# Performance work log

Hardware: AMD Instinct MI355X
Metric: run time of the kernel (lower is better)

## Reference

```python
import jax, jax.numpy as jnp
import numpy as np

B, S, T = 64, 128, 64
HD, VS, VT = 1024, 32000, 32000


def setup_inputs() -> dict:
    key = jax.random.key(0)
    ks = jax.random.split(key, 20)
    p = lambda k, shape: (jax.random.normal(k, shape, jnp.float32) * 0.02)
    return {
        "src_nums": jax.random.randint(ks[0], (B, S), 0, VS, dtype=jnp.int32),
        "tgt_nums": jax.random.randint(ks[1], (B, T), 0, VT, dtype=jnp.int32),
        "src_emb": p(ks[2], (VS, HD)),
        "tgt_emb": p(ks[3], (VT, HD)),
        "enc_Wx1": p(ks[4], (HD, 4 * HD)),
        "enc_Wh1": p(ks[5], (HD, 4 * HD)),
        "enc_b1": jnp.zeros((4 * HD,), jnp.float32),
        "enc_Wx2": p(ks[6], (HD, 4 * HD)),
        "enc_Wh2": p(ks[7], (HD, 4 * HD)),
        "enc_b2": jnp.zeros((4 * HD,), jnp.float32),
        "dec_Wx": p(ks[8], (HD, 4 * HD)),
        "dec_Wh": p(ks[9], (HD, 4 * HD)),
        "dec_b": jnp.zeros((4 * HD,), jnp.float32),
        "dec_h0": p(ks[10], (1, HD)),
        "dec_m0": p(ks[11], (1, HD)),
        "Wt": p(ks[12], (2 * HD, HD)),
        "bt": jnp.zeros((HD,), jnp.float32),
        "Wo": p(ks[13], (HD, VT)),
        "bo": jnp.zeros((VT,), jnp.float32),
    }


def _lstm_cell(x, h, c, Wx, Wh, b):
    g = x @ Wx + h @ Wh + b            # [B, 4H], gate order i,f,g,o
    i, f, gg, o = jnp.split(g, 4, axis=-1)
    c = jax.nn.sigmoid(f) * c + jax.nn.sigmoid(i) * jnp.tanh(gg)
    h = jax.nn.sigmoid(o) * jnp.tanh(c)
    return h, c


def reference(src_nums, tgt_nums, src_emb, tgt_emb,
              enc_Wx1, enc_Wh1, enc_b1, enc_Wx2, enc_Wh2, enc_b2,
              dec_Wx, dec_Wh, dec_b, dec_h0, dec_m0, Wt, bt, Wo, bo):
    Bb, Ss = src_nums.shape
    Hd = src_emb.shape[1]
    # ---- Encoder: 2-layer LSTM over source ----
    embs = src_emb[src_nums]                       # [B,S,H]
    z0 = jnp.zeros((Bb, Hd), embs.dtype)

    def enc_step(carry, x):
        h1, c1, h2, c2 = carry
        h1, c1 = _lstm_cell(x, h1, c1, enc_Wx1, enc_Wh1, enc_b1)
        h2, c2 = _lstm_cell(h1, h2, c2, enc_Wx2, enc_Wh2, enc_b2)
        return (h1, c1, h2, c2), h2

    _, Hseq = jax.lax.scan(enc_step, (z0, z0, z0, z0), jnp.swapaxes(embs, 0, 1))
    Henc = jnp.swapaxes(Hseq, 0, 1)                # [B,S,H]
    mask = src_nums == 0                           # pad mask
    scale = 1.0 / jnp.sqrt(jnp.array(Hd, jnp.float32))

    # ---- Decoder: per-step attention + LSTMCell + tanh proj + log-softmax ----
    h = jnp.tile(dec_h0, (Bb, 1))
    m = jnp.tile(dec_m0, (Bb, 1))

    def dec_step(carry, tgt):
        h, m, loss = carry
        scores = jnp.einsum('bd,bsd->bs', h, Henc) * scale
        scores = jnp.where(mask, -jnp.inf, scores)
        a = jax.nn.softmax(scores, axis=-1)
        ctx = jnp.einsum('bs,bsd->bd', a, Henc)
        z = jnp.tanh(jnp.concatenate([ctx, h], axis=-1) @ Wt + bt)
        logp = jax.nn.log_softmax(z @ Wo + bo, axis=-1)    # [B,V]
        tok_lp = jnp.take_along_axis(logp, tgt[:, None], axis=-1)[:, 0]
        loss = loss - jnp.sum(jnp.where(tgt != 0, tok_lp, 0.0))
        x = tgt_emb[tgt]
        h, m = _lstm_cell(x, h, m, dec_Wx, dec_Wh, dec_b)
        return (h, m, loss), None

    (_, _, loss), _ = jax.lax.scan(
        dec_step, (h, m, jnp.float32(0.0)), jnp.swapaxes(tgt_nums, 0, 1))
    return loss
```

## Files before the change

### kernel.cpp

```cpp
#include <hip/hip_runtime.h>


#define Bv 64
#define Sv 128
#define Tv 64
#define Hv 1024
#define H4v 4096
#define Vv 32000
#define NBLK 256
#define ROUNDS 129

using bf16x8 = __attribute__((ext_vector_type(8))) short;
using f32x4  = __attribute__((ext_vector_type(4))) float;

typedef __attribute__((address_space(1))) const void gvoid_t;
typedef __attribute__((address_space(3))) void lvoid_t;

__device__ __forceinline__ void gload16(const void* g, void* l) {
  __builtin_amdgcn_global_load_lds((gvoid_t*)g, (lvoid_t*)l, 16, 0, 0);
}

__device__ __forceinline__ float bf2f(unsigned short u) {
  unsigned int v = ((unsigned int)u) << 16;
  return __uint_as_float(v);
}
__device__ __forceinline__ unsigned short f2bf(float f) {
  unsigned int u = __float_as_uint(f);
  return (unsigned short)((u + 0x7FFFu + ((u >> 16) & 1u)) >> 16);
}
__device__ __forceinline__ float sigm(float x) { return 1.f / (1.f + __expf(-x)); }
__device__ __forceinline__ float tanh_f(float x) {
  float ax = fabsf(x);
  float e = __expf(-2.f * ax);
  float t = (1.f - e) / (1.f + e);
  return copysignf(t, x);
}

__device__ __forceinline__ int4 ldx4(const unsigned short* p) {
  int4 r;
  asm volatile("global_load_dwordx4 %0, %1, off" : "=v"(r) : "v"(p));
  return r;
}
__device__ __forceinline__ unsigned ldu16(const unsigned short* p) {
  unsigned r;
  asm volatile("global_load_ushort %0, %1, off" : "=v"(r) : "v"(p));
  return r;
}
__device__ __forceinline__ void st_u16_wt(unsigned short* p, unsigned v) {
  asm volatile("global_store_short %0, %1, off sc0 sc1" :: "v"(p), "v"(v) : "memory");
}
__device__ __forceinline__ void vm_wait(int n) {
  if (n >= 8)      asm volatile("s_waitcnt vmcnt(8)" ::: "memory");
  else if (n >= 4) asm volatile("s_waitcnt vmcnt(4)" ::: "memory");
  else             asm volatile("s_waitcnt vmcnt(0)" ::: "memory");
}

__global__ __launch_bounds__(256) void transpose_bf16(const float* __restrict__ in,
                                                      unsigned short* __restrict__ out,
                                                      int R, int C, int ostride) {
  __shared__ float tile[32][33];
  int tx = threadIdx.x, ty = threadIdx.y;
  int c0 = blockIdx.x * 32, r0 = blockIdx.y * 32;
#pragma unroll
  for (int i = 0; i < 32; i += 8)
    tile[ty + i][tx] = in[(size_t)(r0 + ty + i) * C + c0 + tx];
  __syncthreads();
#pragma unroll
  for (int i = 0; i < 32; i += 8)
    out[(size_t)(c0 + ty + i) * ostride + r0 + tx] = f2bf(tile[tx][ty + i]);
}

__global__ __launch_bounds__(256) void gather_emb(const int* __restrict__ toks,
                                                  const float* __restrict__ emb,
                                                  unsigned short* __restrict__ dst) {
  int r = blockIdx.x, tid = threadIdx.x;
  int tok = toks[r];
  int j = tid * 4;
  float4 v = *(const float4*)&emb[(size_t)tok * Hv + j];
  ushort4 o;
  o.x = f2bf(v.x); o.y = f2bf(v.y); o.z = f2bf(v.z); o.w = f2bf(v.w);
  *(ushort4*)&dst[(size_t)r * Hv + j] = o;
}

__global__ __launch_bounds__(256) void init_k(unsigned short* __restrict__ zhx,
                                              unsigned short* __restrict__ hdx0,
                                              const float* __restrict__ h0,
                                              int* __restrict__ bar) {
  int idx = blockIdx.x * 256 + threadIdx.x;
  int j = idx & (Hv - 1);
  int b = idx >> 10;
  zhx[idx] = 0;
  hdx0[(j >> 4) * 1024 + b * 16 + (j & 15)] = f2bf(h0[j]);
  if (idx < 256) bar[idx] = 0;
}

template <int EPI>
__global__ __launch_bounds__(256) void gemm128(const unsigned short* __restrict__ A,
                                               const unsigned short* __restrict__ Bt,
                                               const float* __restrict__ bias,
                                               unsigned short* __restrict__ Cbf,
                                               int M, int N, int K,
                                               float* __restrict__ partial,
                                               float* __restrict__ tlog,
                                               const int* __restrict__ tgt) {
  __shared__ unsigned short As[128 * 64];
  __shared__ unsigned short Bs[128 * 64];
  int tid = threadIdx.x, lane = tid & 63, w = tid >> 6;
  int wr = w >> 1, wc = w & 1;
  int m0 = blockIdx.y * 128, n0 = blockIdx.x * 128;
  f32x4 acc[4][4] = {};
  for (int k0 = 0; k0 < K; k0 += 64) {
    __syncthreads();
#pragma unroll
    for (int q = 0; q < 4; ++q) {
      int idx = q * 256 + tid;
      int row = idx >> 3, phys = idx & 7, lg = phys ^ (row & 7);
      gload16(A + (size_t)(m0 + row) * K + k0 + lg * 8, &As[idx * 8]);
    }
#pragma unroll
    for (int q = 0; q < 4; ++q) {
      int idx = q * 256 + tid;
      int row = idx >> 3, phys = idx & 7, lg = phys ^ (row & 7);
      gload16(Bt + (size_t)(n0 + row) * K + k0 + lg * 8, &Bs[idx * 8]);
    }
    __syncthreads();
#pragma unroll
    for (int kk = 0; kk < 64; kk += 32) {
      int lgb = (kk >> 3) + (lane >> 4);
      bf16x8 af[4], bfr[4];
#pragma unroll
      for (int m = 0; m < 4; ++m) {
        int row = wr * 64 + m * 16 + (lane & 15);
        af[m] = *(const bf16x8*)&As[(row * 8 + (lgb ^ (row & 7))) * 8];
      }
#pragma unroll
      for (int n = 0; n < 4; ++n) {
        int row = wc * 64 + n * 16 + (lane & 15);
        bfr[n] = *(const bf16x8*)&Bs[(row * 8 + (lgb ^ (row & 7))) * 8];
      }
#pragma unroll
      for (int m = 0; m < 4; ++m)
#pragma unroll
        for (int n = 0; n < 4; ++n)
          acc[m][n] = __builtin_amdgcn_mfma_f32_16x16x32_bf16(af[m], bfr[n], acc[m][n], 0, 0, 0);
    }
  }
  if (EPI != 3) {
#pragma unroll
    for (int m = 0; m < 4; ++m)
#pragma unroll
      for (int n = 0; n < 4; ++n) {
        int col = n0 + wc * 64 + n * 16 + (lane & 15);
        float bv = bias[col];
#pragma unroll
        for (int j = 0; j < 4; ++j) {
          int row = m0 + wr * 64 + m * 16 + (lane >> 4) * 4 + j;
          float v = acc[m][n][j] + bv;
          if (EPI == 2) v = tanhf(v);
          Cbf[(size_t)row * N + col] = f2bf(v);
        }
      }
  } else {
    int chunk = (n0 + wc * 64) >> 6;
#pragma unroll
    for (int m = 0; m < 4; ++m)
#pragma unroll
      for (int j = 0; j < 4; ++j) {
        int row = m0 + wr * 64 + m * 16 + (lane >> 4) * 4 + j;
        int tv = tgt[row];
        float se = 0.f;
#pragma unroll
        for (int n = 0; n < 4; ++n) {
          int col = n0 + wc * 64 + n * 16 + (lane & 15);
          float v = acc[m][n][j] + bias[col];
          se += __expf(v);
          if (col == tv) tlog[row] = v;
        }
        se += __shfl_xor(se, 1);
        se += __shfl_xor(se, 2);
        se += __shfl_xor(se, 4);
        se += __shfl_xor(se, 8);
        if ((lane & 15) == 0) partial[(size_t)chunk * M + row] = se;
      }
  }
}

__device__ __forceinline__ void gridbar(int* bar, int target, int tid, int bid) {
  __syncthreads();
  if (tid == 0)
    __hip_atomic_fetch_add(&bar[(bid & 7) * 32], 1, __ATOMIC_RELAXED, __HIP_MEMORY_SCOPE_AGENT);
  if (tid < 8) {
    int it = 0;
    while (true) {
      int s = __hip_atomic_load(&bar[tid * 32], __ATOMIC_RELAXED, __HIP_MEMORY_SCOPE_AGENT);
      s += __shfl_xor(s, 1);
      s += __shfl_xor(s, 2);
      s += __shfl_xor(s, 4);
      if (s >= target) break;
      __builtin_amdgcn_s_sleep(1);
      if (++it > (1 << 18)) break;
    }
  }
  __syncthreads();
}

template <int GRP>
__device__ __forceinline__ void run3(
    int gid, int tid, const unsigned short* __restrict__ Wg,
    const unsigned short* __restrict__ XP, const float* __restrict__ eb2,
    const float* __restrict__ m0, const unsigned short* __restrict__ ZHX,
    unsigned short* __restrict__ H1X, unsigned short* __restrict__ H2X,
    unsigned short* __restrict__ HDX, int* bar,
    unsigned short* Wl, float* gl, int bid) {
  constexpr int COLS = (GRP == 1) ? 8 : 16;
  constexpr int KD   = (GRP == 1) ? 2048 : 1024;
  constexpr int NKS  = KD / 128;
  constexpr int NFR  = (GRP == 1) ? 2 : 4;
  constexpr int TT   = (GRP == 0) ? 128 : 64;
  constexpr int GPR  = KD / 8;
  constexpr int WROWS = 4 * COLS;
  const int lane = tid & 63, w = tid >> 6, l4 = lane >> 4, l15 = lane & 15;
  const int j0 = gid * COLS;

#pragma unroll
  for (int it = 0; it < (WROWS * GPR) / 256; ++it) {
    int L = it * 256 + tid;
    int row = L / GPR;
    int g = (L % GPR) ^ (row & 7);
    int gate = row / COLS, cl = row % COLS;
    gload16(Wg + (size_t)(gate * 1024 + j0 + cl) * KD + g * 8, Wl + (size_t)L * 8);
  }
  const int rr0 = (GRP == 1) ? (tid >> 3) : (tid >> 4);
  const int cc  = (GRP == 1) ? (tid & 7) : (tid & 15);
  const bool cellact = (GRP != 1) || (tid < 128);
  float cst[4];
#pragma unroll
  for (int c = 0; c < 4; ++c) cst[c] = (GRP == 2) ? m0[j0 + cc] : 0.f;
  float br_[4];
  if (GRP == 1) {
#pragma unroll
    for (int g = 0; g < 4; ++g) br_[g] = eb2[g * 1024 + j0 + cc];
  }
  const int kq16 = w * (KD / 32);

  asm volatile("s_waitcnt vmcnt(0)" ::: "memory");
  __syncthreads();

  for (int r = 0; r < ROUNDS; ++r) {
    bool active;
    int t;
    if (GRP == 0)      { active = (r < 128); t = r; }
    else if (GRP == 1) { active = (r >= 1);  t = r - 1; }
    else               { active = (r < 63);  t = r; }
    if (active) {
      const unsigned short* slab;
      int jb;
      if (GRP == 0) {
        slab = (r == 0) ? ZHX : H1X + (size_t)(r - 1) * 65536;
        jb = w * 256;
      } else if (GRP == 2) {
        slab = HDX + (size_t)t * 65536;
        jb = w * 256;
      } else {
        if (w < 2) { slab = H1X + (size_t)(r - 1) * 65536; jb = w * 512; }
        else {
          slab = (t == 0) ? ZHX : H2X + (size_t)(t - 1) * 65536;
          jb = w * 512 - 1024;
        }
      }
      unsigned xgv[16];
      if (GRP != 1) {
#pragma unroll
        for (int c = 0; c < 4; ++c)
#pragma unroll
          for (int g = 0; g < 4; ++g)
            xgv[c * 4 + g] = ldu16(XP + ((size_t)(c * 16 + w * 4 + l4) * TT + t) * H4v +
                                   g * 1024 + j0 + l15);
      }
      const unsigned short* rp[4];
#pragma unroll
      for (int m = 0; m < 4; ++m)
        rp[m] = slab + (size_t)((jb >> 4) + (l4 >> 1)) * 1024 + (m * 16 + l15) * 16 + (l4 & 1) * 8;
      int4 afr[3][4];
#pragma unroll
      for (int pk = 0; pk < 3; ++pk)
#pragma unroll
        for (int m = 0; m < 4; ++m) afr[pk][m] = ldx4(rp[m] + pk * 2048);
      bf16x8 wb[2][NFR];
#pragma unroll
      for (int n = 0; n < NFR; ++n) {
        int row = n * 16 + l15;
        wb[0][n] = *(const bf16x8*)&Wl[(size_t)row * KD + (size_t)((kq16 + l4) ^ (row & 7)) * 8];
      }
      f32x4 acc[4][NFR] = {};
#pragma unroll
      for (int ks = 0; ks < NKS; ++ks) {
        if (ks + 1 < NKS) {
#pragma unroll
          for (int n = 0; n < NFR; ++n) {
            int row = n * 16 + l15;
            wb[(ks + 1) & 1][n] = *(const bf16x8*)&Wl[(size_t)row * KD +
                (size_t)((kq16 + (ks + 1) * 4 + l4) ^ (row & 7)) * 8];
          }
        }
        int nrem = 4 * (NKS - 1 - ks);
        vm_wait(nrem > 8 ? 8 : nrem);
        __builtin_amdgcn_sched_barrier(0);
#pragma unroll
        for (int m = 0; m < 4; ++m)
#pragma unroll
          for (int n = 0; n < NFR; ++n)
            acc[m][n] = __builtin_amdgcn_mfma_f32_16x16x32_bf16(
                *(const bf16x8*)&afr[ks % 3][m], wb[ks & 1][n], acc[m][n], 0, 0, 0);
        if (ks + 3 < NKS) {
#pragma unroll
          for (int m = 0; m < 4; ++m) afr[ks % 3][m] = ldx4(rp[m] + (ks + 3) * 2048);
        }
      }
      unsigned short* outp;
      if (GRP == 0)      outp = H1X + (size_t)r * 65536 + gid * 1024;
      else if (GRP == 2) outp = HDX + (size_t)(t + 1) * 65536 + gid * 1024;
      else               outp = H2X + (size_t)t * 65536 + (size_t)(j0 >> 4) * 1024 + (j0 & 8);
#pragma unroll
      for (int c = 0; c < 4; ++c) {
#pragma unroll
        for (int n = 0; n < NFR; ++n)
#pragma unroll
          for (int j = 0; j < 4; ++j) {
            int ric = l4 * 4 + j;
            int col = n * 16 + l15;
            gl[(w * 16 + ric) * 64 + (col ^ ((ric * 4) & 63))] = acc[c][n][j];
          }
        __syncthreads();
        if (cellact) {
          float G[4];
#pragma unroll
          for (int g = 0; g < 4; ++g) {
            int sw = (g * COLS + cc) ^ ((rr0 * 4) & 63);
            G[g] = gl[(0 * 16 + rr0) * 64 + sw] + gl[(1 * 16 + rr0) * 64 + sw] +
                   gl[(2 * 16 + rr0) * 64 + sw] + gl[(3 * 16 + rr0) * 64 + sw];
          }
          float gi, gf, gg, go;
          if (GRP == 1) {
            gi = G[0] + br_[0]; gf = G[1] + br_[1]; gg = G[2] + br_[2]; go = G[3] + br_[3];
          } else {
            gi = G[0] + bf2f((unsigned short)xgv[c * 4 + 0]);
            gf = G[1] + bf2f((unsigned short)xgv[c * 4 + 1]);
            gg = G[2] + bf2f((unsigned short)xgv[c * 4 + 2]);
            go = G[3] + bf2f((unsigned short)xgv[c * 4 + 3]);
          }
          float cn = sigm(gf) * cst[c] + sigm(gi) * tanh_f(gg);
          float hn = sigm(go) * tanh_f(cn);
          cst[c] = cn;
          st_u16_wt(outp + (c * 16 + rr0) * 16 + cc, (unsigned)f2bf(hn));
        }
        __syncthreads();
      }
      asm volatile("s_waitcnt vmcnt(0)" ::: "memory");
    }
    if (r + 1 < ROUNDS) gridbar(bar, NBLK * (r + 1), tid, bid);
  }
}

__global__ __launch_bounds__(256, 1) void chain_kernel(
    const unsigned short* __restrict__ W1T, const unsigned short* __restrict__ W2S,
    const unsigned short* __restrict__ WDT, const unsigned short* __restrict__ XP1,
    const unsigned short* __restrict__ XPD, const float* __restrict__ eb2,
    const float* __restrict__ m0, const unsigned short* __restrict__ ZHX,
    unsigned short* __restrict__ H1X, unsigned short* __restrict__ H2X,
    unsigned short* __restrict__ HDX, int* bar) {
  __shared__ unsigned short Wl[65536];
  __shared__ float gl[4 * 16 * 64];
  int bid = blockIdx.x, tid = threadIdx.x;
  if (bid < 64)
    run3<0>(bid, tid, W1T, XP1, eb2, m0, ZHX, H1X, H2X, HDX, bar, Wl, gl, bid);
  else if (bid < 192)
    run3<1>(bid - 64, tid, W2S, nullptr, eb2, m0, ZHX, H1X, H2X, HDX, bar, Wl, gl, bid);
  else
    run3<2>(bid - 192, tid, WDT, XPD, eb2, m0, ZHX, H1X, H2X, HDX, bar, Wl, gl, bid);
}

__global__ __launch_bounds__(256) void reshape_h(const unsigned short* __restrict__ H2X,
                                                 const unsigned short* __restrict__ HDX,
                                                 unsigned short* __restrict__ HENC,
                                                 unsigned short* __restrict__ HDEC) {
  int row = blockIdx.x, tid = threadIdx.x;
  int g = tid >> 2, c = (tid & 3) * 4;
  if (row < Bv * Sv) {
    int b = row >> 7, s = row & 127;
    ushort4 v = *(const ushort4*)&H2X[(size_t)s * 65536 + g * 1024 + b * 16 + c];
    *(ushort4*)&HENC[(size_t)row * Hv + tid * 4] = v;
  } else {
    int r2 = row - Bv * Sv;
    int b = r2 >> 6, t = r2 & 63;
    ushort4 v = *(const ushort4*)&HDX[(size_t)t * 65536 + g * 1024 + b * 16 + c];
    *(ushort4*)&HDEC[(size_t)r2 * Hv + tid * 4] = v;
  }
}

__global__ __launch_bounds__(256) void attn_kernel(const unsigned short* __restrict__ Hdec,
                                                   const unsigned short* __restrict__ Henc,
                                                   const int* __restrict__ src_nums,
                                                   unsigned short* __restrict__ cat) {
  __shared__ float hd[Hv];
  __shared__ float sc[Sv];
  __shared__ float al[Sv];
  __shared__ float inv_s;
  int r = blockIdx.x;
  int b = r >> 6;
  int tid = threadIdx.x;
#pragma unroll
  for (int i = 0; i < 4; ++i) {
    int j = i * 256 + tid;
    hd[j] = bf2f(Hdec[(size_t)r * Hv + j]);
  }
  __syncthreads();
  int lane = tid & 63, w = tid >> 6;
  {
    int s = w * 32 + (lane >> 1);
    int half = lane & 1;
    const unsigned short* hrow = Henc + ((size_t)(b * Sv + s)) * Hv + half * 512;
    const float* hdp = hd + half * 512;
    float ps = 0.f;
#pragma unroll 8
    for (int j = 0; j < 512; j += 2) {
      unsigned int u = *(const unsigned int*)&hrow[j];
      ps += hdp[j] * bf2f((unsigned short)(u & 0xFFFFu));
      ps += hdp[j + 1] * bf2f((unsigned short)(u >> 16));
    }
    ps += __shfl_xor(ps, 1);
    if (half == 0) {
      float v = ps * 0.03125f;
      if (src_nums[b * Sv + s] == 0) v = -1e30f;
      sc[s] = v;
    }
  }
  __syncthreads();
  if (w == 0) {
    float v0 = sc[lane], v1 = sc[lane + 64];
    float mx = fmaxf(v0, v1);
#pragma unroll
    for (int o = 1; o < 64; o <<= 1) mx = fmaxf(mx, __shfl_xor(mx, o));
    float e0 = __expf(v0 - mx), e1 = __expf(v1 - mx);
    al[lane] = e0;
    al[lane + 64] = e1;
    float ss = e0 + e1;
#pragma unroll
    for (int o = 1; o < 64; o <<= 1) ss += __shfl_xor(ss, o);
    if (lane == 0) inv_s = 1.f / ss;
  }
  __syncthreads();
  float inv = inv_s;
  int j0 = tid * 4;
  float a0 = 0, a1 = 0, a2 = 0, a3 = 0;
  for (int s2 = 0; s2 < Sv; ++s2) {
    float a = al[s2];
    const unsigned short* hr = Henc + ((size_t)(b * Sv + s2)) * Hv + j0;
    ushort4 u = *(const ushort4*)hr;
    a0 += a * bf2f(u.x);
    a1 += a * bf2f(u.y);
    a2 += a * bf2f(u.z);
    a3 += a * bf2f(u.w);
  }
  ushort4 o4;
  o4.x = f2bf(a0 * inv); o4.y = f2bf(a1 * inv); o4.z = f2bf(a2 * inv); o4.w = f2bf(a3 * inv);
  *(ushort4*)&cat[(size_t)r * 2048 + j0] = o4;
  ushort4 h4;
  h4.x = f2bf(hd[j0]); h4.y = f2bf(hd[j0 + 1]); h4.z = f2bf(hd[j0 + 2]); h4.w = f2bf(hd[j0 + 3]);
  *(ushort4*)&cat[(size_t)r * 2048 + 1024 + j0] = h4;
}

__global__ __launch_bounds__(256) void loss_row(const float* __restrict__ partial,
                                                const float* __restrict__ tlog,
                                                const int* __restrict__ tgt,
                                                float* __restrict__ rowloss) {
  int r = blockIdx.x * 256 + threadIdx.x;
  float ssum = 0.f;
  for (int c = 0; c < Vv / 64; ++c) ssum += partial[(size_t)c * (Bv * Tv) + r];
  float l = logf(ssum) - tlog[r];
  rowloss[r] = (tgt[r] != 0) ? l : 0.f;
}

__global__ __launch_bounds__(256) void loss_final(const float* __restrict__ rowloss,
                                                  float* __restrict__ out) {
  __shared__ float red[256];
  int tid = threadIdx.x;
  float s = 0.f;
  for (int i = tid; i < Bv * Tv; i += 256) s += rowloss[i];
  red[tid] = s;
  __syncthreads();
  for (int o = 128; o > 0; o >>= 1) {
    if (tid < o) red[tid] += red[tid + o];
    __syncthreads();
  }
  if (tid == 0) out[0] = red[0];
}

extern "C" void kernel_launch(void* const* d_in, const int* in_sizes, int n_in,
                              void* d_out, int out_size, void* d_ws, size_t ws_size,
                              hipStream_t stream) {
  (void)in_sizes; (void)n_in; (void)out_size; (void)ws_size;
  const int* src_nums = (const int*)d_in[0];
  const int* tgt_nums = (const int*)d_in[1];
  const float* src_emb = (const float*)d_in[2];
  const float* tgt_emb = (const float*)d_in[3];
  const float* eWx1 = (const float*)d_in[4];
  const float* eWh1 = (const float*)d_in[5];
  const float* eb1  = (const float*)d_in[6];
  const float* eWx2 = (const float*)d_in[7];
  const float* eWh2 = (const float*)d_in[8];
  const float* eb2  = (const float*)d_in[9];
  const float* dWx  = (const float*)d_in[10];
  const float* dWh  = (const float*)d_in[11];
  const float* db   = (const float*)d_in[12];
  const float* h0   = (const float*)d_in[13];
  const float* m0   = (const float*)d_in[14];
  const float* Wt   = (const float*)d_in[15];
  const float* bt   = (const float*)d_in[16];
  const float* Wo   = (const float*)d_in[17];
  const float* bo   = (const float*)d_in[18];

  char* base = (char*)d_ws;
  size_t off = 0;
  auto alloc = [&](size_t bytes) -> void* {
    void* r = base + off;
    off += (bytes + 255) & ~(size_t)255;
    return r;
  };
  unsigned short* WX1T = (unsigned short*)alloc((size_t)H4v * Hv * 2);
  unsigned short* W1T  = (unsigned short*)alloc((size_t)H4v * Hv * 2);
  unsigned short* W2S  = (unsigned short*)alloc((size_t)H4v * 2048 * 2);
  unsigned short* DWXT = (unsigned short*)alloc((size_t)H4v * Hv * 2);
  unsigned short* WDT  = (unsigned short*)alloc((size_t)H4v * Hv * 2);
  unsigned short* WTT  = (unsigned short*)alloc((size_t)Hv * 2048 * 2);
  unsigned short* WOT  = (unsigned short*)alloc((size_t)Vv * Hv * 2);
  unsigned short* SEMB = (unsigned short*)alloc((size_t)Bv * Sv * Hv * 2);
  unsigned short* TEMB = (unsigned short*)alloc((size_t)Bv * Tv * Hv * 2);
  unsigned short* XP1  = (unsigned short*)alloc((size_t)Bv * Sv * H4v * 2);
  unsigned short* XPD  = (unsigned short*)alloc((size_t)Bv * Tv * H4v * 2);
  unsigned short* HENC = (unsigned short*)alloc((size_t)Bv * Sv * Hv * 2);
  unsigned short* HDEC = (unsigned short*)alloc((size_t)Bv * Tv * Hv * 2);
  unsigned short* H1X  = (unsigned short*)alloc((size_t)Sv * Bv * Hv * 2);
  unsigned short* H2X  = (unsigned short*)alloc((size_t)Sv * Bv * Hv * 2);
  unsigned short* HDX  = (unsigned short*)alloc((size_t)Tv * Bv * Hv * 2);
  unsigned short* ZHX  = (unsigned short*)alloc((size_t)Bv * Hv * 2);
  unsigned short* CAT  = (unsigned short*)alloc((size_t)Bv * Tv * 2048 * 2);
  unsigned short* ZBUF = (unsigned short*)alloc((size_t)Bv * Tv * Hv * 2);
  float* PART  = (float*)alloc((size_t)(Vv / 64) * (Bv * Tv) * 4);
  float* TLOG  = (float*)alloc((size_t)(Bv * Tv) * 4);
  float* RLOSS = (float*)alloc((size_t)(Bv * Tv) * 4);
  int* BAR     = (int*)alloc(256 * 4);

  dim3 tb(32, 8);
  transpose_bf16<<<dim3(H4v / 32, Hv / 32), tb, 0, stream>>>(eWx1, WX1T, Hv, H4v, Hv);
  transpose_bf16<<<dim3(H4v / 32, Hv / 32), tb, 0, stream>>>(eWh1, W1T, Hv, H4v, Hv);
  transpose_bf16<<<dim3(H4v / 32, Hv / 32), tb, 0, stream>>>(eWx2, W2S, Hv, H4v, 2048);
  transpose_bf16<<<dim3(H4v / 32, Hv / 32), tb, 0, stream>>>(eWh2, W2S + 1024, Hv, H4v, 2048);
  transpose_bf16<<<dim3(H4v / 32, Hv / 32), tb, 0, stream>>>(dWx, DWXT, Hv, H4v, Hv);
  transpose_bf16<<<dim3(H4v / 32, Hv / 32), tb, 0, stream>>>(dWh, WDT, Hv, H4v, Hv);
  transpose_bf16<<<dim3(Hv / 32, 2048 / 32), tb, 0, stream>>>(Wt, WTT, 2048, Hv, 2048);
  transpose_bf16<<<dim3(Vv / 32, Hv / 32), tb, 0, stream>>>(Wo, WOT, Hv, Vv, Hv);

  init_k<<<256, 256, 0, stream>>>(ZHX, HDX, h0, BAR);
  gather_emb<<<Bv * Sv, 256, 0, stream>>>(src_nums, src_emb, SEMB);
  gather_emb<<<Bv * Tv, 256, 0, stream>>>(tgt_nums, tgt_emb, TEMB);

  gemm128<1><<<dim3(H4v / 128, (Bv * Sv) / 128), 256, 0, stream>>>(
      SEMB, WX1T, eb1, XP1, Bv * Sv, H4v, Hv, nullptr, nullptr, nullptr);
  gemm128<1><<<dim3(H4v / 128, (Bv * Tv) / 128), 256, 0, stream>>>(
      TEMB, DWXT, db, XPD, Bv * Tv, H4v, Hv, nullptr, nullptr, nullptr);

  chain_kernel<<<NBLK, 256, 0, stream>>>(W1T, W2S, WDT, XP1, XPD, eb2, m0, ZHX, H1X, H2X, HDX, BAR);

  reshape_h<<<Bv * Sv + Bv * Tv, 256, 0, stream>>>(H2X, HDX, HENC, HDEC);

  attn_kernel<<<Bv * Tv, 256, 0, stream>>>(HDEC, HENC, src_nums, CAT);
  gemm128<2><<<dim3(Hv / 128, (Bv * Tv) / 128), 256, 0, stream>>>(
      CAT, WTT, bt, ZBUF, Bv * Tv, Hv, 2048, nullptr, nullptr, nullptr);
  gemm128<3><<<dim3(Vv / 128, (Bv * Tv) / 128), 256, 0, stream>>>(
      ZBUF, WOT, bo, nullptr, Bv * Tv, Vv, Hv, PART, TLOG, tgt_nums);
  loss_row<<<(Bv * Tv) / 256, 256, 0, stream>>>(PART, TLOG, tgt_nums, RLOSS);
  loss_final<<<1, 256, 0, stream>>>(RLOSS, (float*)d_out);
}
```

Measured before the change: 1.891 ms.

## Replace grid barriers with per-step dataflow counters and pack input-projection gates

The persistent LSTM chain kernel no longer runs a global barrier every round. Each group now waits only on per-timestep counters posted by its producers, so layer 1, layer 2 and the decoder can run as a pipeline instead of in lockstep. The input-projection GEMM epilogue writes gate values in a packed per-(t, column-block, batch) layout, so each cell reads its four gate biases with one 8-byte load instead of sixteen scattered 2-byte loads. The risks are relaxed-atomic ordering and visibility, and a larger counter array to initialise.

```diff
diff --git a/kernel.cpp b/kernel.cpp
--- a/kernel.cpp
+++ b/kernel.cpp
@@ -8,7 +8,6 @@
 #define H4v 4096
 #define Vv 32000
 #define NBLK 256
-#define ROUNDS 129
 
 using bf16x8 = __attribute__((ext_vector_type(8))) short;
 using f32x4  = __attribute__((ext_vector_type(4))) float;
@@ -41,18 +40,35 @@
   asm volatile("global_load_dwordx4 %0, %1, off" : "=v"(r) : "v"(p));
   return r;
 }
-__device__ __forceinline__ unsigned ldu16(const unsigned short* p) {
-  unsigned r;
-  asm volatile("global_load_ushort %0, %1, off" : "=v"(r) : "v"(p));
+__device__ __forceinline__ int2 ldx2(const unsigned short* p) {
+  int2 r;
+  asm volatile("global_load_dwordx2 %0, %1, off" : "=v"(r) : "v"(p));
   return r;
 }
 __device__ __forceinline__ void st_u16_wt(unsigned short* p, unsigned v) {
   asm volatile("global_store_short %0, %1, off sc0 sc1" :: "v"(p), "v"(v) : "memory");
 }
 __device__ __forceinline__ void vm_wait(int n) {
-  if (n >= 8)      asm volatile("s_waitcnt vmcnt(8)" ::: "memory");
+  if (n >= 12)     asm volatile("s_waitcnt vmcnt(12)" ::: "memory");
+  else if (n >= 8) asm volatile("s_waitcnt vmcnt(8)" ::: "memory");
   else if (n >= 4) asm volatile("s_waitcnt vmcnt(4)" ::: "memory");
   else             asm volatile("s_waitcnt vmcnt(0)" ::: "memory");
+}
+
+__device__ __forceinline__ void wait_cnt(int* c, int target, int tid) {
+  if (tid == 0) {
+    int it = 0;
+    while (__hip_atomic_load(c, __ATOMIC_RELAXED, __HIP_MEMORY_SCOPE_AGENT) < target) {
+      __builtin_amdgcn_s_sleep(1);
+      if (++it > (1 << 20)) break;
+    }
+  }
+  __syncthreads();
+}
+__device__ __forceinline__ void post_cnt(int* c, int tid) {
+  __syncthreads();
+  if (tid == 0)
+    __hip_atomic_fetch_add(c, 1, __ATOMIC_RELAXED, __HIP_MEMORY_SCOPE_AGENT);
 }
 
 __global__ __launch_bounds__(256) void transpose_bf16(const float* __restrict__ in,
@@ -85,13 +101,13 @@
 __global__ __launch_bounds__(256) void init_k(unsigned short* __restrict__ zhx,
                                               unsigned short* __restrict__ hdx0,
                                               const float* __restrict__ h0,
-                                              int* __restrict__ bar) {
+                                              int* __restrict__ cnt) {
   int idx = blockIdx.x * 256 + threadIdx.x;
   int j = idx & (Hv - 1);
   int b = idx >> 10;
   zhx[idx] = 0;
   hdx0[(j >> 4) * 1024 + b * 16 + (j & 15)] = f2bf(h0[j]);
-  if (idx < 256) bar[idx] = 0;
+  if (idx < 6144) cnt[idx] = 0;
 }
 
 template <int EPI>
@@ -145,7 +161,7 @@
           acc[m][n] = __builtin_amdgcn_mfma_f32_16x16x32_bf16(af[m], bfr[n], acc[m][n], 0, 0, 0);
     }
   }
-  if (EPI != 3) {
+  if (EPI == 2) {
 #pragma unroll
     for (int m = 0; m < 4; ++m)
 #pragma unroll
@@ -156,11 +172,10 @@
         for (int j = 0; j < 4; ++j) {
           int row = m0 + wr * 64 + m * 16 + (lane >> 4) * 4 + j;
           float v = acc[m][n][j] + bv;
-          if (EPI == 2) v = tanhf(v);
-          Cbf[(size_t)row * N + col] = f2bf(v);
+          Cbf[(size_t)row * N + col] = f2bf(tanhf(v));
         }
       }
-  } else {
+  } else if (EPI == 3) {
     int chunk = (n0 + wc * 64) >> 6;
 #pragma unroll
     for (int m = 0; m < 4; ++m)
@@ -182,41 +197,40 @@
         se += __shfl_xor(se, 8);
         if ((lane & 15) == 0) partial[(size_t)chunk * M + row] = se;
       }
-  }
-}
-
-__device__ __forceinline__ void gridbar(int* bar, int target, int tid, int bid) {
-  __syncthreads();
-  if (tid == 0)
-    __hip_atomic_fetch_add(&bar[(bid & 7) * 32], 1, __ATOMIC_RELAXED, __HIP_MEMORY_SCOPE_AGENT);
-  if (tid < 8) {
-    int it = 0;
-    while (true) {
-      int s = __hip_atomic_load(&bar[tid * 32], __ATOMIC_RELAXED, __HIP_MEMORY_SCOPE_AGENT);
-      s += __shfl_xor(s, 1);
-      s += __shfl_xor(s, 2);
-      s += __shfl_xor(s, 4);
-      if (s >= target) break;
-      __builtin_amdgcn_s_sleep(1);
-      if (++it > (1 << 18)) break;
-    }
-  }
-  __syncthreads();
+  } else {
+    constexpr int TTc = (EPI == 4) ? 128 : 64;
+#pragma unroll
+    for (int m = 0; m < 4; ++m)
+#pragma unroll
+      for (int n = 0; n < 4; ++n) {
+        int col = n0 + wc * 64 + n * 16 + (lane & 15);
+        float bv = bias[col];
+        int hcol = col & 1023, g = col >> 10;
+#pragma unroll
+        for (int j = 0; j < 4; ++j) {
+          int row = m0 + wr * 64 + m * 16 + (lane >> 4) * 4 + j;
+          int t = row % TTc, b = row / TTc;
+          float v = acc[m][n][j] + bv;
+          Cbf[((((size_t)t * 64 + (hcol >> 4)) * 64 + b) * 16 + (hcol & 15)) * 4 + g] = f2bf(v);
+        }
+      }
+  }
 }
 
 template <int GRP>
-__device__ __forceinline__ void run3(
+__device__ __forceinline__ void run4(
     int gid, int tid, const unsigned short* __restrict__ Wg,
-    const unsigned short* __restrict__ XP, const float* __restrict__ eb2,
+    const unsigned short* __restrict__ XPC, const float* __restrict__ eb2,
     const float* __restrict__ m0, const unsigned short* __restrict__ ZHX,
     unsigned short* __restrict__ H1X, unsigned short* __restrict__ H2X,
-    unsigned short* __restrict__ HDX, int* bar,
-    unsigned short* Wl, float* gl, int bid) {
+    unsigned short* __restrict__ HDX,
+    int* __restrict__ C1, int* __restrict__ C2, int* __restrict__ CD,
+    unsigned short* Wl, float* gl) {
   constexpr int COLS = (GRP == 1) ? 8 : 16;
   constexpr int KD   = (GRP == 1) ? 2048 : 1024;
   constexpr int NKS  = KD / 128;
   constexpr int NFR  = (GRP == 1) ? 2 : 4;
-  constexpr int TT   = (GRP == 0) ? 128 : 64;
+  constexpr int NT   = (GRP == 2) ? 63 : 128;
   constexpr int GPR  = KD / 8;
   constexpr int WROWS = 4 * COLS;
   const int lane = tid & 63, w = tid >> 6, l4 = lane >> 4, l15 = lane & 15;
@@ -246,138 +260,143 @@
   asm volatile("s_waitcnt vmcnt(0)" ::: "memory");
   __syncthreads();
 
-  for (int r = 0; r < ROUNDS; ++r) {
-    bool active;
-    int t;
-    if (GRP == 0)      { active = (r < 128); t = r; }
-    else if (GRP == 1) { active = (r >= 1);  t = r - 1; }
-    else               { active = (r < 63);  t = r; }
-    if (active) {
-      const unsigned short* slab;
-      int jb;
-      if (GRP == 0) {
-        slab = (r == 0) ? ZHX : H1X + (size_t)(r - 1) * 65536;
-        jb = w * 256;
-      } else if (GRP == 2) {
-        slab = HDX + (size_t)t * 65536;
-        jb = w * 256;
-      } else {
-        if (w < 2) { slab = H1X + (size_t)(r - 1) * 65536; jb = w * 512; }
-        else {
-          slab = (t == 0) ? ZHX : H2X + (size_t)(t - 1) * 65536;
-          jb = w * 512 - 1024;
+  for (int t = 0; t < NT; ++t) {
+    if (GRP == 0) {
+      if (t > 0) wait_cnt(C1 + (t - 1) * 16, 64, tid);
+    } else if (GRP == 1) {
+      wait_cnt(C1 + t * 16, 64, tid);
+      if (t > 0) wait_cnt(C2 + (t - 1) * 16, 128, tid);
+    } else {
+      if (t > 0) wait_cnt(CD + t * 16, 64, tid);
+    }
+    const unsigned short* slab;
+    int jb;
+    if (GRP == 0) {
+      slab = (t == 0) ? ZHX : H1X + (size_t)(t - 1) * 65536;
+      jb = w * 256;
+    } else if (GRP == 2) {
+      slab = HDX + (size_t)t * 65536;
+      jb = w * 256;
+    } else {
+      if (w < 2) { slab = H1X + (size_t)t * 65536; jb = w * 512; }
+      else {
+        slab = (t == 0) ? ZHX : H2X + (size_t)(t - 1) * 65536;
+        jb = w * 512 - 1024;
+      }
+    }
+    int2 xq[4];
+    if (GRP != 1) {
+      const unsigned short* xb = XPC + (((size_t)t * 64 + gid) * 64) * 64;
+#pragma unroll
+      for (int c = 0; c < 4; ++c)
+        xq[c] = ldx2(xb + ((c * 16 + rr0) * 16 + cc) * 4);
+    }
+    const unsigned short* rp[4];
+#pragma unroll
+    for (int m = 0; m < 4; ++m)
+      rp[m] = slab + (size_t)((jb >> 4) + (l4 >> 1)) * 1024 + (m * 16 + l15) * 16 + (l4 & 1) * 8;
+    int4 afr[3][4];
+#pragma unroll
+    for (int pk = 0; pk < 3; ++pk)
+#pragma unroll
+      for (int m = 0; m < 4; ++m) afr[pk][m] = ldx4(rp[m] + pk * 2048);
+    if (GRP != 1) vm_wait(12);
+    bf16x8 wb[2][NFR];
+#pragma unroll
+    for (int n = 0; n < NFR; ++n) {
+      int row = n * 16 + l15;
+      wb[0][n] = *(const bf16x8*)&Wl[(size_t)row * KD + (size_t)((kq16 + l4) ^ (row & 7)) * 8];
+    }
+    f32x4 acc[4][NFR] = {};
+#pragma unroll
+    for (int ks = 0; ks < NKS; ++ks) {
+      if (ks + 1 < NKS) {
+#pragma unroll
+        for (int n = 0; n < NFR; ++n) {
+          int row = n * 16 + l15;
+          wb[(ks + 1) & 1][n] = *(const bf16x8*)&Wl[(size_t)row * KD +
+              (size_t)((kq16 + (ks + 1) * 4 + l4) ^ (row & 7)) * 8];
         }
       }
-      unsigned xgv[16];
-      if (GRP != 1) {
-#pragma unroll
-        for (int c = 0; c < 4; ++c)
-#pragma unroll
-          for (int g = 0; g < 4; ++g)
-            xgv[c * 4 + g] = ldu16(XP + ((size_t)(c * 16 + w * 4 + l4) * TT + t) * H4v +
-                                   g * 1024 + j0 + l15);
-      }
-      const unsigned short* rp[4];
+      int nrem = 4 * (NKS - 1 - ks);
+      vm_wait(nrem > 8 ? 8 : nrem);
+      __builtin_amdgcn_sched_barrier(0);
 #pragma unroll
       for (int m = 0; m < 4; ++m)
-        rp[m] = slab + (size_t)((jb >> 4) + (l4 >> 1)) * 1024 + (m * 16 + l15) * 16 + (l4 & 1) * 8;
-      int4 afr[3][4];
-#pragma unroll
-      for (int pk = 0; pk < 3; ++pk)
-#pragma unroll
-        for (int m = 0; m < 4; ++m) afr[pk][m] = ldx4(rp[m] + pk * 2048);
-      bf16x8 wb[2][NFR];
-#pragma unroll
-      for (int n = 0; n < NFR; ++n) {
-        int row = n * 16 + l15;
-        wb[0][n] = *(const bf16x8*)&Wl[(size_t)row * KD + (size_t)((kq16 + l4) ^ (row & 7)) * 8];
-      }
-      f32x4 acc[4][NFR] = {};
-#pragma unroll
-      for (int ks = 0; ks < NKS; ++ks) {
-        if (ks + 1 < NKS) {
-#pragma unroll
-          for (int n = 0; n < NFR; ++n) {
-            int row = n * 16 + l15;
-            wb[(ks + 1) & 1][n] = *(const bf16x8*)&Wl[(size_t)row * KD +
-                (size_t)((kq16 + (ks + 1) * 4 + l4) ^ (row & 7)) * 8];
-          }
+#pragma unroll
+        for (int n = 0; n < NFR; ++n)
+          acc[m][n] = __builtin_amdgcn_mfma_f32_16x16x32_bf16(
+              *(const bf16x8*)&afr[ks % 3][m], wb[ks & 1][n], acc[m][n], 0, 0, 0);
+      if (ks + 3 < NKS) {
+#pragma unroll
+        for (int m = 0; m < 4; ++m) afr[ks % 3][m] = ldx4(rp[m] + (ks + 3) * 2048);
+      }
+    }
+    unsigned short* outp;
+    if (GRP == 0)      outp = H1X + (size_t)t * 65536 + gid * 1024;
+    else if (GRP == 2) outp = HDX + (size_t)(t + 1) * 65536 + gid * 1024;
+    else               outp = H2X + (size_t)t * 65536 + (size_t)(j0 >> 4) * 1024 + (j0 & 8);
+#pragma unroll
+    for (int c = 0; c < 4; ++c) {
+#pragma unroll
+      for (int n = 0; n < NFR; ++n)
+#pragma unroll
+        for (int j = 0; j < 4; ++j) {
+          int ric = l4 * 4 + j;
+          int col = n * 16 + l15;
+          gl[(w * 16 + ric) * 64 + (col ^ ((ric * 4) & 63))] = acc[c][n][j];
         }
-        int nrem = 4 * (NKS - 1 - ks);
-        vm_wait(nrem > 8 ? 8 : nrem);
-        __builtin_amdgcn_sched_barrier(0);
-#pragma unroll
-        for (int m = 0; m < 4; ++m)
-#pragma unroll
-          for (int n = 0; n < NFR; ++n)
-            acc[m][n] = __builtin_amdgcn_mfma_f32_16x16x32_bf16(
-                *(const bf16x8*)&afr[ks % 3][m], wb[ks & 1][n], acc[m][n], 0, 0, 0);
-        if (ks + 3 < NKS) {
-#pragma unroll
-          for (int m = 0; m < 4; ++m) afr[ks % 3][m] = ldx4(rp[m] + (ks + 3) * 2048);
+      __syncthreads();
+      if (cellact) {
+        float G[4];
+#pragma unroll
+        for (int g = 0; g < 4; ++g) {
+          int sw = (g * COLS + cc) ^ ((rr0 * 4) & 63);
+          G[g] = gl[(0 * 16 + rr0) * 64 + sw] + gl[(1 * 16 + rr0) * 64 + sw] +
+                 gl[(2 * 16 + rr0) * 64 + sw] + gl[(3 * 16 + rr0) * 64 + sw];
         }
-      }
-      unsigned short* outp;
-      if (GRP == 0)      outp = H1X + (size_t)r * 65536 + gid * 1024;
-      else if (GRP == 2) outp = HDX + (size_t)(t + 1) * 65536 + gid * 1024;
-      else               outp = H2X + (size_t)t * 65536 + (size_t)(j0 >> 4) * 1024 + (j0 & 8);
-#pragma unroll
-      for (int c = 0; c < 4; ++c) {
-#pragma unroll
-        for (int n = 0; n < NFR; ++n)
-#pragma unroll
-          for (int j = 0; j < 4; ++j) {
-            int ric = l4 * 4 + j;
-            int col = n * 16 + l15;
-            gl[(w * 16 + ric) * 64 + (col ^ ((ric * 4) & 63))] = acc[c][n][j];
-          }
-        __syncthreads();
-        if (cellact) {
-          float G[4];
-#pragma unroll
-          for (int g = 0; g < 4; ++g) {
-            int sw = (g * COLS + cc) ^ ((rr0 * 4) & 63);
-            G[g] = gl[(0 * 16 + rr0) * 64 + sw] + gl[(1 * 16 + rr0) * 64 + sw] +
-                   gl[(2 * 16 + rr0) * 64 + sw] + gl[(3 * 16 + rr0) * 64 + sw];
-          }
-          float gi, gf, gg, go;
-          if (GRP == 1) {
-            gi = G[0] + br_[0]; gf = G[1] + br_[1]; gg = G[2] + br_[2]; go = G[3] + br_[3];
-          } else {
-            gi = G[0] + bf2f((unsigned short)xgv[c * 4 + 0]);
-            gf = G[1] + bf2f((unsigned short)xgv[c * 4 + 1]);
-            gg = G[2] + bf2f((unsigned short)xgv[c * 4 + 2]);
-            go = G[3] + bf2f((unsigned short)xgv[c * 4 + 3]);
-          }
-          float cn = sigm(gf) * cst[c] + sigm(gi) * tanh_f(gg);
-          float hn = sigm(go) * tanh_f(cn);
-          cst[c] = cn;
-          st_u16_wt(outp + (c * 16 + rr0) * 16 + cc, (unsigned)f2bf(hn));
+        float gi, gf, gg, go;
+        if (GRP == 1) {
+          gi = G[0] + br_[0]; gf = G[1] + br_[1]; gg = G[2] + br_[2]; go = G[3] + br_[3];
+        } else {
+          gi = G[0] + bf2f((unsigned short)(xq[c].x & 0xFFFF));
+          gf = G[1] + bf2f((unsigned short)((unsigned)xq[c].x >> 16));
+          gg = G[2] + bf2f((unsigned short)(xq[c].y & 0xFFFF));
+          go = G[3] + bf2f((unsigned short)((unsigned)xq[c].y >> 16));
         }
-        __syncthreads();
-      }
-      asm volatile("s_waitcnt vmcnt(0)" ::: "memory");
-    }
-    if (r + 1 < ROUNDS) gridbar(bar, NBLK * (r + 1), tid, bid);
+        float cn = sigm(gf) * cst[c] + sigm(gi) * tanh_f(gg);
+        float hn = sigm(go) * tanh_f(cn);
+        cst[c] = cn;
+        st_u16_wt(outp + (c * 16 + rr0) * 16 + cc, (unsigned)f2bf(hn));
+      }
+      __syncthreads();
+    }
+    asm volatile("s_waitcnt vmcnt(0)" ::: "memory");
+    if (GRP == 0)      post_cnt(C1 + t * 16, tid);
+    else if (GRP == 1) post_cnt(C2 + t * 16, tid);
+    else               post_cnt(CD + (t + 1) * 16, tid);
   }
 }
 
 __global__ __launch_bounds__(256, 1) void chain_kernel(
     const unsigned short* __restrict__ W1T, const unsigned short* __restrict__ W2S,
-    const unsigned short* __restrict__ WDT, const unsigned short* __restrict__ XP1,
-    const unsigned short* __restrict__ XPD, const float* __restrict__ eb2,
+    const unsigned short* __restrict__ WDT, const unsigned short* __restrict__ XPC1,
+    const unsigned short* __restrict__ XPCD, const float* __restrict__ eb2,
     const float* __restrict__ m0, const unsigned short* __restrict__ ZHX,
     unsigned short* __restrict__ H1X, unsigned short* __restrict__ H2X,
-    unsigned short* __restrict__ HDX, int* bar) {
+    unsigned short* __restrict__ HDX, int* __restrict__ cnt) {
   __shared__ unsigned short Wl[65536];
   __shared__ float gl[4 * 16 * 64];
   int bid = blockIdx.x, tid = threadIdx.x;
+  int* C1 = cnt;
+  int* C2 = cnt + 160 * 16;
+  int* CD = cnt + 320 * 16;
   if (bid < 64)
-    run3<0>(bid, tid, W1T, XP1, eb2, m0, ZHX, H1X, H2X, HDX, bar, Wl, gl, bid);
+    run4<0>(bid, tid, W1T, XPC1, eb2, m0, ZHX, H1X, H2X, HDX, C1, C2, CD, Wl, gl);
   else if (bid < 192)
-    run3<1>(bid - 64, tid, W2S, nullptr, eb2, m0, ZHX, H1X, H2X, HDX, bar, Wl, gl, bid);
+    run4<1>(bid - 64, tid, W2S, nullptr, eb2, m0, ZHX, H1X, H2X, HDX, C1, C2, CD, Wl, gl);
   else
-    run3<2>(bid - 192, tid, WDT, XPD, eb2, m0, ZHX, H1X, H2X, HDX, bar, Wl, gl, bid);
+    run4<2>(bid - 192, tid, WDT, XPCD, eb2, m0, ZHX, H1X, H2X, HDX, C1, C2, CD, Wl, gl);
 }
 
 __global__ __launch_bounds__(256) void reshape_h(const unsigned short* __restrict__ H2X,
@@ -536,8 +555,8 @@
   unsigned short* WOT  = (unsigned short*)alloc((size_t)Vv * Hv * 2);
   unsigned short* SEMB = (unsigned short*)alloc((size_t)Bv * Sv * Hv * 2);
   unsigned short* TEMB = (unsigned short*)alloc((size_t)Bv * Tv * Hv * 2);
-  unsigned short* XP1  = (unsigned short*)alloc((size_t)Bv * Sv * H4v * 2);
-  unsigned short* XPD  = (unsigned short*)alloc((size_t)Bv * Tv * H4v * 2);
+  unsigned short* XPC1 = (unsigned short*)alloc((size_t)Bv * Sv * H4v * 2);
+  unsigned short* XPCD = (unsigned short*)alloc((size_t)Bv * Tv * H4v * 2);
   unsigned short* HENC = (unsigned short*)alloc((size_t)Bv * Sv * Hv * 2);
   unsigned short* HDEC = (unsigned short*)alloc((size_t)Bv * Tv * Hv * 2);
   unsigned short* H1X  = (unsigned short*)alloc((size_t)Sv * Bv * Hv * 2);
@@ -549,7 +568,7 @@
   float* PART  = (float*)alloc((size_t)(Vv / 64) * (Bv * Tv) * 4);
   float* TLOG  = (float*)alloc((size_t)(Bv * Tv) * 4);
   float* RLOSS = (float*)alloc((size_t)(Bv * Tv) * 4);
-  int* BAR     = (int*)alloc(256 * 4);
+  int* CNT     = (int*)alloc(6144 * 4);
 
   dim3 tb(32, 8);
   transpose_bf16<<<dim3(H4v / 32, Hv / 32), tb, 0, stream>>>(eWx1, WX1T, Hv, H4v, Hv);
@@ -561,16 +580,17 @@
   transpose_bf16<<<dim3(Hv / 32, 2048 / 32), tb, 0, stream>>>(Wt, WTT, 2048, Hv, 2048);
   transpose_bf16<<<dim3(Vv / 32, Hv / 32), tb, 0, stream>>>(Wo, WOT, Hv, Vv, Hv);
 
-  init_k<<<256, 256, 0, stream>>>(ZHX, HDX, h0, BAR);
+  init_k<<<256, 256, 0, stream>>>(ZHX, HDX, h0, CNT);
   gather_emb<<<Bv * Sv, 256, 0, stream>>>(src_nums, src_emb, SEMB);
   gather_emb<<<Bv * Tv, 256, 0, stream>>>(tgt_nums, tgt_emb, TEMB);
 
-  gemm128<1><<<dim3(H4v / 128, (Bv * Sv) / 128), 256, 0, stream>>>(
-      SEMB, WX1T, eb1, XP1, Bv * Sv, H4v, Hv, nullptr, nullptr, nullptr);
-  gemm128<1><<<dim3(H4v / 128, (Bv * Tv) / 128), 256, 0, stream>>>(
-      TEMB, DWXT, db, XPD, Bv * Tv, H4v, Hv, nullptr, nullptr, nullptr);
-
-  chain_kernel<<<NBLK, 256, 0, stream>>>(W1T, W2S, WDT, XP1, XPD, eb2, m0, ZHX, H1X, H2X, HDX, BAR);
+  gemm128<4><<<dim3(H4v / 128, (Bv * Sv) / 128), 256, 0, stream>>>(
+      SEMB, WX1T, eb1, XPC1, Bv * Sv, H4v, Hv, nullptr, nullptr, nullptr);
+  gemm128<5><<<dim3(H4v / 128, (Bv * Tv) / 128), 256, 0, stream>>>(
+      TEMB, DWXT, db, XPCD, Bv * Tv, H4v, Hv, nullptr, nullptr, nullptr);
+
+  chain_kernel<<<NBLK, 256, 0, stream>>>(W1T, W2S, WDT, XPC1, XPCD, eb2, m0, ZHX, H1X, H2X,
+                                         HDX, CNT);
 
   reshape_h<<<Bv * Sv + Bv * Tv, 256, 0, stream>>>(H2X, HDX, HENC, HDEC);
 
```

After: 1.828 ms. 1.03x faster.
